# Performance work log

Hardware: AMD Instinct MI355X
Metric: run time of the kernel (lower is better)

The kernel has to match this reference:

```python
import jax, jax.numpy as jnp
import numpy as np

N_HEAD = 16
N_KV_HEAD = 8
HEAD_DIM = 128
BLOCK_SIZE = 2048


def _rope_cache(T, hd):
    # faithful to torch: freqs repeat_interleave(2) along last dim
    inv_freq = 1.0 / (10000.0 ** (jnp.arange(0, hd, 2, dtype=jnp.float32) / hd))
    t = jnp.arange(T, dtype=jnp.float32)
    freqs = jnp.outer(t, inv_freq)            # [T, hd/2]
    freqs = jnp.repeat(freqs, 2, axis=-1)     # [T, hd]
    return jnp.cos(freqs), jnp.sin(freqs)


def _apply_rope(x, cos, sin):
    # x: [B, H, T, hd]; rotate-half convention from the torch code
    hd = x.shape[-1]
    x1, x2 = x[..., : hd // 2], x[..., hd // 2 :]
    x_rot = jnp.concatenate([-x2, x1], axis=-1)
    return x * cos + x_rot * sin


def setup_inputs() -> dict:
    key = jax.random.key(0)
    ks = jax.random.split(key, 5)
    B, T, C = 4, 2048, 2048
    kv_dim = N_KV_HEAD * HEAD_DIM
    s = 0.02
    return {
        "x": jax.random.normal(ks[0], (B, T, C), dtype=jnp.float32),
        "Wq": jax.random.normal(ks[1], (C, C), dtype=jnp.float32) * s,
        "Wk": jax.random.normal(ks[2], (kv_dim, C), dtype=jnp.float32) * s,
        "Wv": jax.random.normal(ks[3], (kv_dim, C), dtype=jnp.float32) * s,
        "Wo": jax.random.normal(ks[4], (C, C), dtype=jnp.float32) * s,
    }


def reference(x, Wq, Wk, Wv, Wo):
    B, T, C = x.shape
    hd = HEAD_DIM
    # projections (torch Linear: x @ W.T)
    q = (x @ Wq.T).reshape(B, T, N_HEAD, hd).transpose(0, 2, 1, 3)      # [B,H,T,hd]
    k = (x @ Wk.T).reshape(B, T, N_KV_HEAD, hd).transpose(0, 2, 1, 3)   # [B,Hkv,T,hd]
    v = (x @ Wv.T).reshape(B, T, N_KV_HEAD, hd).transpose(0, 2, 1, 3)

    cos, sin = _rope_cache(T, hd)  # start_pos = 0
    q = _apply_rope(q, cos, sin)
    k = _apply_rope(k, cos, sin)

    # GQA: repeat kv heads
    rep = N_HEAD // N_KV_HEAD
    k = jnp.repeat(k, rep, axis=1)  # [B,H,T,hd]
    v = jnp.repeat(v, rep, axis=1)

    scale = 1.0 / jnp.sqrt(jnp.float32(hd))
    scores = jnp.einsum("bhqd,bhkd->bhqk", q, k) * scale
    causal = jnp.tril(jnp.ones((T, T), dtype=bool))
    scores = jnp.where(causal, scores, jnp.finfo(scores.dtype).min)
    attn = jax.nn.softmax(scores, axis=-1)
    out = jnp.einsum("bhqk,bhkd->bhqd", attn, v)  # [B,H,T,hd]

    y = out.transpose(0, 2, 1, 3).reshape(B, T, C)
    return y @ Wo.T
```

## Files before the change

kernel.cpp:

```cpp
#include <hip/hip_runtime.h>

#define SCALE 0.08838834764831845f

typedef unsigned short bfu;
typedef __attribute__((ext_vector_type(8))) short bf16x8;
typedef __attribute__((ext_vector_type(4))) float f32x4;
typedef __attribute__((ext_vector_type(16))) float f32x16;

__device__ __forceinline__ unsigned short f2bf(float f) {
  unsigned int u = __float_as_uint(f);
  u += 0x7FFFu + ((u >> 16) & 1u);
  return (unsigned short)(u >> 16);
}
__device__ __forceinline__ float bf2f(unsigned short h) {
  return __uint_as_float(((unsigned int)h) << 16);
}
__device__ __forceinline__ unsigned int cvtpk(float a, float b) {
  unsigned int r;
  asm("v_cvt_pk_bf16_f32 %0, %1, %2" : "=v"(r) : "v"(a), "v"(b));
  return r;
}
__device__ __forceinline__ void async16(const void* g, void* l) {
  __builtin_amdgcn_global_load_lds(
      (const __attribute__((address_space(1))) unsigned int*)g,
      (__attribute__((address_space(3))) unsigned int*)l, 16, 0, 0);
}
__device__ __forceinline__ void barrier_sb() {
  __builtin_amdgcn_sched_barrier(0);
  __builtin_amdgcn_s_barrier();
  __builtin_amdgcn_sched_barrier(0);
}
__device__ __forceinline__ void wait4_bar() {
  __builtin_amdgcn_sched_barrier(0);
  asm volatile("s_waitcnt vmcnt(4)" ::: "memory");
  __builtin_amdgcn_s_barrier();
  __builtin_amdgcn_sched_barrier(0);
}
__device__ __forceinline__ void wait0_bar() {
  __builtin_amdgcn_sched_barrier(0);
  asm volatile("s_waitcnt vmcnt(0)" ::: "memory");
  __builtin_amdgcn_s_barrier();
  __builtin_amdgcn_sched_barrier(0);
}

__global__ __launch_bounds__(256) void cvt_bf16(const float* __restrict__ src,
                                                bfu* __restrict__ dst, int n4) {
  int i = blockIdx.x * 256 + threadIdx.x;
  if (i >= n4) return;
  float4 v = ((const float4*)src)[i];
  ushort4 o;
  o.x = f2bf(v.x); o.y = f2bf(v.y); o.z = f2bf(v.z); o.w = f2bf(v.w);
  ((ushort4*)dst)[i] = o;
}

__global__ __launch_bounds__(256) void rope_table(float2* __restrict__ tab) {
  int idx = blockIdx.x * 256 + threadIdx.x;
  int t = idx >> 6, f = idx & 63;
  const float nl = -0.14391156463f;
  float th = (float)t * expf((float)f * nl);
  tab[idx] = make_float2(cosf(th), sinf(th));
}

__device__ __forceinline__ void storeC(float* p, float v) { *p = v; }
__device__ __forceinline__ void storeC(bfu* p, float v) { *p = f2bf(v); }

template <typename OutT, bool FUSE>
__global__ __launch_bounds__(512, 2) void gemm256(
    const bfu* __restrict__ A, const bfu* __restrict__ B,
    OutT* __restrict__ C, const float2* __restrict__ ropeTab,
    bfu* __restrict__ qTo, bfu* __restrict__ kTo, bfu* __restrict__ vTo,
    int M, int N, int K) {
  __shared__ __align__(16) char smem[131072];
  const int tid = threadIdx.x;
  const int w = tid >> 6, l = tid & 63;
  const int lr = l & 15, lg = l >> 4;
  const int wr = w >> 2, wc = w & 3;

  const int nwg = gridDim.x * gridDim.y;
  const int flat = blockIdx.y * gridDim.x + blockIdx.x;
  const int swz = (flat & 7) * (nwg >> 3) + (flat >> 3);
  const int m0 = (swz % gridDim.x) * 256;
  const int n0 = (swz / gridDim.x) * 256;

  const int sr = l >> 3;
  const int sc = (l & 7) ^ sr;
  auto stageHalf = [&](const bfu* G, int grow0, int kcol, char* lds) {
#pragma unroll
    for (int j = 0; j < 2; j++) {
      int row = (j * 8 + w) * 8 + sr;
      async16(G + (size_t)(grow0 + row) * K + kcol + sc * 8,
              lds + (j * 8 + w) * 1024 + l * 16);
    }
  };

  f32x4 acc[8][4];
#pragma unroll
  for (int i = 0; i < 8; i++)
#pragma unroll
    for (int j = 0; j < 4; j++) acc[i][j] = (f32x4){0.f, 0.f, 0.f, 0.f};

  stageHalf(A, m0, 0, smem);
  stageHalf(A, m0 + 128, 0, smem + 16384);
  stageHalf(B, n0, 0, smem + 65536);
  stageHalf(B, n0 + 128, 0, smem + 65536 + 16384);

  const int KT = K >> 6;
  const int swiz = (lr & 7) << 4;
  const int cbase = (wc >> 1) * 128 + (wc & 1) * 32;
#pragma unroll 1
  for (int t = 0; t < KT; t++) {
    const int bt = t & 1;
    const char* Ah = smem + bt * 32768 + wr * 16384;
    const char* Bt = smem + 65536 + bt * 32768;
    char* An = smem + (bt ^ 1) * 32768;
    char* Bn = smem + 65536 + (bt ^ 1) * 32768;
    const bool pfch = (t + 1 < KT);
    const int kn = (t + 1) << 6;

    if (pfch) {
      stageHalf(A, m0, kn, An);
      asm volatile("s_waitcnt vmcnt(2)" ::: "memory");
    } else {
      asm volatile("s_waitcnt vmcnt(0)" ::: "memory");
    }
    barrier_sb();

    bf16x8 bfr[4][2];
#pragma unroll
    for (int n = 0; n < 4; n++) {
      const char* rowp =
          Bt + (cbase + (n & 1) * 16 + (n >> 1) * 64 + lr) * 128;
#pragma unroll
      for (int s = 0; s < 2; s++)
        bfr[n][s] = *(const bf16x8*)(rowp + ((((s << 2) + lg) << 4) ^ swiz));
    }

#pragma unroll
    for (int p = 0; p < 4; p++) {
      bf16x8 af[2][2];
#pragma unroll
      for (int m2 = 0; m2 < 2; m2++) {
        const char* rowp = Ah + ((p * 2 + m2) * 16 + lr) * 128;
#pragma unroll
        for (int s = 0; s < 2; s++)
          af[m2][s] = *(const bf16x8*)(rowp + ((((s << 2) + lg) << 4) ^ swiz));
      }
      if (pfch) {
        if (p == 1) stageHalf(A, m0 + 128, kn, An + 16384);
        if (p == 2) stageHalf(B, n0, kn, Bn);
        if (p == 3) stageHalf(B, n0 + 128, kn, Bn + 16384);
      }
      __builtin_amdgcn_s_setprio(1);
#pragma unroll
      for (int m2 = 0; m2 < 2; m2++)
#pragma unroll
        for (int n = 0; n < 4; n++)
#pragma unroll
          for (int s = 0; s < 2; s++)
            acc[p * 2 + m2][n] = __builtin_amdgcn_mfma_f32_16x16x32_bf16(
                af[m2][s], bfr[n][s], acc[p * 2 + m2][n], 0, 0, 0);
      __builtin_amdgcn_s_setprio(0);
    }
    barrier_sb();
  }

  if constexpr (!FUSE) {
#pragma unroll
    for (int i = 0; i < 8; i++)
#pragma unroll
      for (int j = 0; j < 4; j++)
#pragma unroll
        for (int r = 0; r < 4; r++) {
          int gm = m0 + wr * 128 + i * 16 + lg * 4 + r;
          int gn = n0 + cbase + (j & 1) * 16 + (j >> 1) * 64 + lr;
          storeC(&C[(size_t)gm * N + gn], acc[i][j][r]);
        }
  } else {
    const int head = (n0 >> 7) + (wc >> 1);
    if (head < 24) {
#pragma unroll
      for (int i = 0; i < 8; i++)
#pragma unroll
        for (int r = 0; r < 4; r++) {
          int gm = m0 + wr * 128 + i * 16 + lg * 4 + r;
          int tt = gm & 2047, bb = gm >> 11;
          bfu* rowp = (head < 16)
                          ? qTo + (((size_t)((bb * 16 + head) * 2048 + tt)) << 7)
                          : kTo + (((size_t)((bb * 8 + head - 16) * 2048 + tt)) << 7);
          const float2* trow = ropeTab + tt * 64;
#pragma unroll
          for (int n = 0; n < 2; n++) {
            int d = (wc & 1) * 32 + n * 16 + lr;
            int i1 = d >> 1;
            float2 cs1 = trow[i1];
            float2 cs2 = trow[i1 + 32];
            float x1 = acc[i][n][r], x2 = acc[i][n + 2][r];
            rowp[d] = f2bf(x1 * cs1.x - x2 * cs1.y);
            rowp[d + 64] = f2bf(x2 * cs2.x + x1 * cs2.y);
          }
        }
    } else {
      const int kh = head - 24;
#pragma unroll
      for (int i = 0; i < 8; i++) {
        int gm0 = m0 + wr * 128 + i * 16 + lg * 4;
        int t0 = gm0 & 2047, bb = gm0 >> 11;
#pragma unroll
        for (int n = 0; n < 4; n++) {
          int d = (wc & 1) * 32 + (n & 1) * 16 + (n >> 1) * 64 + lr;
          bfu* p = vTo + (((size_t)((bb * 8 + kh) * 128 + d)) << 11) + t0;
          ushort4 o;
          o.x = f2bf(acc[i][n][0]);
          o.y = f2bf(acc[i][n][1]);
          o.z = f2bf(acc[i][n][2]);
          o.w = f2bf(acc[i][n][3]);
          *(ushort4*)p = o;
        }
      }
    }
  }
}

__global__ __launch_bounds__(256, 3) void flash_attn5(const bfu* __restrict__ qT,
                                                      const bfu* __restrict__ kT,
                                                      const bfu* __restrict__ vT,
                                                      bfu* __restrict__ attn) {
  __shared__ __align__(16) char smem[49152];
  const int tid = threadIdx.x;
  const int w = tid >> 6, l = tid & 63;
  const int ln = l & 31, h2 = l >> 5;
  const int idx = blockIdx.x;
  const int khb = idx & 31;
  const int hs = (idx >> 5) & 1;
  const int qt = 15 - (idx >> 6);
  const int kh = khb & 7, b = khb >> 3;
  const int hh = kh * 2 + hs;
  const int NT = 2 * qt + 2;
  const int qrow0 = qt * 128 + w * 32;
  const int myrow = qrow0 + ln;

  const bfu* Qh = qT + ((size_t)(b * 16 + hh) * 2048) * 128;
  const bfu* Kb = kT + ((size_t)(b * 8 + kh) * 2048) * 128;
  const bfu* Vb = vT + ((size_t)(b * 8 + kh) * 128) * 2048;

  auto stageK = [&](int kbuf, int t) {
    char* Kl = smem + kbuf * 16384;
    const bfu* src = Kb + (size_t)t * 64 * 128;
#pragma unroll
    for (int ii = 0; ii < 4; ii++) {
      int i = w * 4 + ii;
      int row = i * 4 + (l >> 4);
      int ck = (l & 15) ^ (row & 15);
      async16(src + row * 128 + ck * 8, Kl + i * 1024 + l * 16);
    }
  };
  auto stageV = [&](int t) {
    char* Vl = smem + 32768;
    const bfu* src = Vb + t * 64;
#pragma unroll
    for (int jj = 0; jj < 4; jj++) {
      int j = w * 4 + jj;
      int row = j * 8 + (l >> 3);
      int ck = (l & 7) ^ (row & 7);
      async16(src + (size_t)row * 2048 + ck * 8, Vl + j * 1024 + l * 16);
    }
  };

  bf16x8 qf[8];
#pragma unroll
  for (int dt = 0; dt < 8; dt++)
    qf[dt] = *(const bf16x8*)(Qh + (size_t)myrow * 128 + dt * 16 + h2 * 8);

  f32x16 O[4];
#pragma unroll
  for (int mt = 0; mt < 4; mt++)
#pragma unroll
    for (int r = 0; r < 16; r++) O[mt][r] = 0.f;
  float li = 0.f;

  stageK(0, 0);
  stageV(0);
  wait4_bar();

  int kb = 0;
#pragma unroll 1
  for (int t = 0; t < NT; t++) {
    const bool pf = (t + 1 < NT);
    if (pf) stageK(kb ^ 1, t + 1);

    const int k0 = t * 64;
    const bool active = k0 <= qrow0 + 31;
    bf16x8 pfr[4];

    if (active) {
      const char* Kl = smem + kb * 16384;
      f32x16 S0, S1;
#pragma unroll
      for (int r = 0; r < 16; r++) { S0[r] = 0.f; S1[r] = 0.f; }
      const int swk = (ln & 15) << 4;
      __builtin_amdgcn_s_setprio(1);
#pragma unroll
      for (int dt = 0; dt < 8; dt++) {
        bf16x8 kf0 =
            *(const bf16x8*)(Kl + ln * 256 + ((dt * 32 + h2 * 16) ^ swk));
        bf16x8 kf1 = *(const bf16x8*)(Kl + (32 + ln) * 256 +
                                      ((dt * 32 + h2 * 16) ^ swk));
        S0 = __builtin_amdgcn_mfma_f32_32x32x16_bf16(kf0, qf[dt], S0, 0, 0, 0);
        S1 = __builtin_amdgcn_mfma_f32_32x32x16_bf16(kf1, qf[dt], S1, 0, 0, 0);
      }
      __builtin_amdgcn_s_setprio(0);

      const bool need_mask = (k0 + 63) > qrow0;
#pragma unroll
      for (int half = 0; half < 2; half++) {
        float p[16];
#pragma unroll
        for (int r = 0; r < 16; r++) {
          float s = half ? S1[r] : S0[r];
          float pv = __builtin_exp2f(fmaf(s, 0.12751743f, -17.312340f));
          if (need_mask) {
            int key = k0 + half * 32 + (r & 3) + 8 * (r >> 2) + 4 * h2;
            if (key > myrow) pv = 0.f;
          }
          p[r] = pv;
          li += pv;
        }
#pragma unroll
        for (int kt = 0; kt < 2; kt++) {
          const float* q = p + kt * 8;
          unsigned int lo0 = cvtpk(q[0], q[1]);
          unsigned int lo1 = cvtpk(q[2], q[3]);
          unsigned int hi0 = cvtpk(q[4], q[5]);
          unsigned int hi1 = cvtpk(q[6], q[7]);
          unsigned int plo0 = __shfl_xor((int)lo0, 32);
          unsigned int plo1 = __shfl_xor((int)lo1, 32);
          unsigned int phi0 = __shfl_xor((int)hi0, 32);
          unsigned int phi1 = __shfl_xor((int)hi1, 32);
          union { unsigned int u[4]; bf16x8 v; } c;
          c.u[0] = h2 ? phi0 : lo0;
          c.u[1] = h2 ? phi1 : lo1;
          c.u[2] = h2 ? hi0 : plo0;
          c.u[3] = h2 ? hi1 : plo1;
          pfr[half * 2 + kt] = c.v;
        }
      }
    }

    if (pf) wait4_bar(); else wait0_bar();

    if (active) {
      const char* Vl = smem + 32768;
      const int swv = (ln & 7) << 4;
      __builtin_amdgcn_s_setprio(1);
#pragma unroll
      for (int mt = 0; mt < 4; mt++) {
        const char* vb = Vl + (mt * 32 + ln) * 128;
#pragma unroll
        for (int kt = 0; kt < 4; kt++) {
          bf16x8 vf = *(const bf16x8*)(vb + ((kt * 32 + h2 * 16) ^ swv));
          O[mt] = __builtin_amdgcn_mfma_f32_32x32x16_bf16(vf, pfr[kt], O[mt], 0, 0, 0);
        }
      }
      __builtin_amdgcn_s_setprio(0);
    }

    if (pf) {
      wait0_bar();
      stageV(t + 1);
    }
    kb ^= 1;
  }

  li += __shfl_xor(li, 32);
  const float inv = 1.f / li;
  bfu* orow = attn + ((size_t)(b * 2048 + qrow0 + ln)) * 2048 + hh * 128;
#pragma unroll
  for (int mt = 0; mt < 4; mt++)
#pragma unroll
    for (int g = 0; g < 4; g++) {
      unsigned int r0 = cvtpk(O[mt][g * 4 + 0] * inv, O[mt][g * 4 + 1] * inv);
      unsigned int r1 = cvtpk(O[mt][g * 4 + 2] * inv, O[mt][g * 4 + 3] * inv);
      uint2 o; o.x = r0; o.y = r1;
      *(uint2*)(orow + mt * 32 + g * 8 + h2 * 4) = o;
    }
}

extern "C" void kernel_launch(void* const* d_in, const int* in_sizes, int n_in,
                              void* d_out, int out_size, void* d_ws, size_t ws_size,
                              hipStream_t stream) {
  const float* x = (const float*)d_in[0];
  const float* Wq = (const float*)d_in[1];
  const float* Wk = (const float*)d_in[2];
  const float* Wv = (const float*)d_in[3];
  const float* Wo = (const float*)d_in[4];
  float* out = (float*)d_out;
  char* ws = (char*)d_ws;

  bfu* xb     = (bfu*)(ws);
  bfu* Wqkv   = (bfu*)(ws + 33554432);
  bfu* Wob    = (bfu*)(ws + 50331648);
  float2* tab = (float2*)(ws + 58720256);
  bfu* qT     = (bfu*)(ws + 125829120);
  bfu* kT     = (bfu*)(ws + 159383552);
  bfu* vT     = (bfu*)(ws + 176160768);
  bfu* attn = xb;

  cvt_bf16<<<16384, 256, 0, stream>>>(x, xb, 4194304);
  cvt_bf16<<<4096, 256, 0, stream>>>(Wq, Wqkv, 1048576);
  cvt_bf16<<<2048, 256, 0, stream>>>(Wk, Wqkv + (size_t)2048 * 2048, 524288);
  cvt_bf16<<<2048, 256, 0, stream>>>(Wv, Wqkv + (size_t)3072 * 2048, 524288);
  cvt_bf16<<<4096, 256, 0, stream>>>(Wo, Wob, 1048576);
  rope_table<<<512, 256, 0, stream>>>(tab);

  gemm256<bfu, true><<<dim3(32, 16), 512, 0, stream>>>(
      xb, Wqkv, (bfu*)nullptr, tab, qT, kT, vT, 8192, 4096, 2048);
  flash_attn5<<<1024, 256, 0, stream>>>(qT, kT, vT, attn);
  gemm256<float, false><<<dim3(32, 8), 512, 0, stream>>>(
      attn, Wob, out, nullptr, nullptr, nullptr, nullptr, 8192, 2048, 2048);
}
```

Before: 488.9 us.

## Pair causal q-tiles per block and share K/V tiles across both GQA heads

The attention kernel now uses 512-thread blocks in which both query heads of a KV group share each staged K/V tile. Each block processes q-tile pg and then q-tile 15-pg back to back, which evens out the causal work so every block runs 34 iterations. K and V are now double-buffered together and refilled with a single wait/barrier per iteration. The lane-32 shuffles are replaced with v_permlane32_swap. The changes target redundant K/V loads, causal load imbalance and synchronisation stalls, at the cost of more LDS per block and only 256 blocks in the grid.

After: 453.5 us. -7.2%, faster.

```diff
diff --git a/kernel.cpp b/kernel.cpp
--- a/kernel.cpp
+++ b/kernel.cpp
@@ -20,6 +20,9 @@
   asm("v_cvt_pk_bf16_f32 %0, %1, %2" : "=v"(r) : "v"(a), "v"(b));
   return r;
 }
+__device__ __forceinline__ void pl32swap(unsigned int& a, unsigned int& b) {
+  asm volatile("v_permlane32_swap_b32 %0, %1" : "+v"(a), "+v"(b));
+}
 __device__ __forceinline__ void async16(const void* g, void* l) {
   __builtin_amdgcn_global_load_lds(
       (const __attribute__((address_space(1))) unsigned int*)g,
@@ -27,12 +30,6 @@
 }
 __device__ __forceinline__ void barrier_sb() {
   __builtin_amdgcn_sched_barrier(0);
-  __builtin_amdgcn_s_barrier();
-  __builtin_amdgcn_sched_barrier(0);
-}
-__device__ __forceinline__ void wait4_bar() {
-  __builtin_amdgcn_sched_barrier(0);
-  asm volatile("s_waitcnt vmcnt(4)" ::: "memory");
   __builtin_amdgcn_s_barrier();
   __builtin_amdgcn_sched_barrier(0);
 }
@@ -221,55 +218,56 @@
   }
 }
 
-__global__ __launch_bounds__(256, 3) void flash_attn5(const bfu* __restrict__ qT,
+__global__ __launch_bounds__(512, 2) void flash_attn7(const bfu* __restrict__ qT,
                                                       const bfu* __restrict__ kT,
                                                       const bfu* __restrict__ vT,
                                                       bfu* __restrict__ attn) {
-  __shared__ __align__(16) char smem[49152];
+  __shared__ __align__(16) char smem[65536];
   const int tid = threadIdx.x;
   const int w = tid >> 6, l = tid & 63;
   const int ln = l & 31, h2 = l >> 5;
+  const int hsw = w >> 2, w4 = w & 3;
   const int idx = blockIdx.x;
   const int khb = idx & 31;
-  const int hs = (idx >> 5) & 1;
-  const int qt = 15 - (idx >> 6);
+  const int pg = idx >> 5;
   const int kh = khb & 7, b = khb >> 3;
-  const int hh = kh * 2 + hs;
-  const int NT = 2 * qt + 2;
-  const int qrow0 = qt * 128 + w * 32;
-  const int myrow = qrow0 + ln;
+  const int hh = kh * 2 + hsw;
+  const int nkbA = 2 * pg + 2;
+  const int NT = 34;
 
   const bfu* Qh = qT + ((size_t)(b * 16 + hh) * 2048) * 128;
   const bfu* Kb = kT + ((size_t)(b * 8 + kh) * 2048) * 128;
   const bfu* Vb = vT + ((size_t)(b * 8 + kh) * 128) * 2048;
 
-  auto stageK = [&](int kbuf, int t) {
-    char* Kl = smem + kbuf * 16384;
+  auto stageK = [&](int buf, int t) {
+    char* Kl = smem + buf * 16384;
     const bfu* src = Kb + (size_t)t * 64 * 128;
 #pragma unroll
-    for (int ii = 0; ii < 4; ii++) {
-      int i = w * 4 + ii;
+    for (int ii = 0; ii < 2; ii++) {
+      int i = w * 2 + ii;
       int row = i * 4 + (l >> 4);
       int ck = (l & 15) ^ (row & 15);
       async16(src + row * 128 + ck * 8, Kl + i * 1024 + l * 16);
     }
   };
-  auto stageV = [&](int t) {
-    char* Vl = smem + 32768;
+  auto stageV = [&](int buf, int t) {
+    char* Vl = smem + 32768 + buf * 16384;
     const bfu* src = Vb + t * 64;
 #pragma unroll
-    for (int jj = 0; jj < 4; jj++) {
-      int j = w * 4 + jj;
+    for (int jj = 0; jj < 2; jj++) {
+      int j = w * 2 + jj;
       int row = j * 8 + (l >> 3);
       int ck = (l & 7) ^ (row & 7);
       async16(src + (size_t)row * 2048 + ck * 8, Vl + j * 1024 + l * 16);
     }
   };
 
+  int qrow0 = pg * 128 + w4 * 32;
+
   bf16x8 qf[8];
 #pragma unroll
   for (int dt = 0; dt < 8; dt++)
-    qf[dt] = *(const bf16x8*)(Qh + (size_t)myrow * 128 + dt * 16 + h2 * 8);
+    qf[dt] = *(const bf16x8*)(Qh + (size_t)(qrow0 + ln) * 128 + dt * 16 + h2 * 8);
 
   f32x16 O[4];
 #pragma unroll
@@ -278,22 +276,53 @@
     for (int r = 0; r < 16; r++) O[mt][r] = 0.f;
   float li = 0.f;
 
+  auto flush = [&]() {
+    float ls = li + __shfl_xor(li, 32);
+    float inv = 1.f / ls;
+    bfu* orow = attn + ((size_t)(b * 2048 + qrow0 + ln)) * 2048 + hh * 128;
+#pragma unroll
+    for (int mt = 0; mt < 4; mt++)
+#pragma unroll
+      for (int g = 0; g < 4; g++) {
+        unsigned int r0 = cvtpk(O[mt][g * 4 + 0] * inv, O[mt][g * 4 + 1] * inv);
+        unsigned int r1 = cvtpk(O[mt][g * 4 + 2] * inv, O[mt][g * 4 + 3] * inv);
+        uint2 o; o.x = r0; o.y = r1;
+        *(uint2*)(orow + mt * 32 + g * 8 + h2 * 4) = o;
+      }
+  };
+
   stageK(0, 0);
-  stageV(0);
-  wait4_bar();
-
-  int kb = 0;
+  stageV(0, 0);
+
 #pragma unroll 1
   for (int t = 0; t < NT; t++) {
-    const bool pf = (t + 1 < NT);
-    if (pf) stageK(kb ^ 1, t + 1);
-
-    const int k0 = t * 64;
-    const bool active = k0 <= qrow0 + 31;
-    bf16x8 pfr[4];
-
-    if (active) {
-      const char* Kl = smem + kb * 16384;
+    wait0_bar();
+    if (t + 1 < NT) {
+      const int kn = (t + 1 >= nkbA) ? (t + 1 - nkbA) : (t + 1);
+      stageK((t + 1) & 1, kn);
+      stageV((t + 1) & 1, kn);
+    }
+
+    if (t == nkbA) {
+      flush();
+      qrow0 = (15 - pg) * 128 + w4 * 32;
+#pragma unroll
+      for (int dt = 0; dt < 8; dt++)
+        qf[dt] =
+            *(const bf16x8*)(Qh + (size_t)(qrow0 + ln) * 128 + dt * 16 + h2 * 8);
+#pragma unroll
+      for (int mt = 0; mt < 4; mt++)
+#pragma unroll
+        for (int r = 0; r < 16; r++) O[mt][r] = 0.f;
+      li = 0.f;
+    }
+
+    const int k0 = ((t >= nkbA) ? (t - nkbA) : t) * 64;
+    const int myrow = qrow0 + ln;
+    if (k0 <= qrow0 + 31) {
+      const char* Kl = smem + (t & 1) * 16384;
+      const char* Vl = smem + 32768 + (t & 1) * 16384;
+
       f32x16 S0, S1;
 #pragma unroll
       for (int r = 0; r < 16; r++) { S0[r] = 0.f; S1[r] = 0.f; }
@@ -311,6 +340,7 @@
       __builtin_amdgcn_s_setprio(0);
 
       const bool need_mask = (k0 + 63) > qrow0;
+      bf16x8 pfr[4];
 #pragma unroll
       for (int half = 0; half < 2; half++) {
         float p[16];
@@ -328,28 +358,18 @@
 #pragma unroll
         for (int kt = 0; kt < 2; kt++) {
           const float* q = p + kt * 8;
-          unsigned int lo0 = cvtpk(q[0], q[1]);
-          unsigned int lo1 = cvtpk(q[2], q[3]);
-          unsigned int hi0 = cvtpk(q[4], q[5]);
-          unsigned int hi1 = cvtpk(q[6], q[7]);
-          unsigned int plo0 = __shfl_xor((int)lo0, 32);
-          unsigned int plo1 = __shfl_xor((int)lo1, 32);
-          unsigned int phi0 = __shfl_xor((int)hi0, 32);
-          unsigned int phi1 = __shfl_xor((int)hi1, 32);
+          unsigned int a0 = cvtpk(q[0], q[1]);
+          unsigned int a1 = cvtpk(q[2], q[3]);
+          unsigned int b0 = cvtpk(q[4], q[5]);
+          unsigned int b1 = cvtpk(q[6], q[7]);
+          pl32swap(a0, b0);
+          pl32swap(a1, b1);
           union { unsigned int u[4]; bf16x8 v; } c;
-          c.u[0] = h2 ? phi0 : lo0;
-          c.u[1] = h2 ? phi1 : lo1;
-          c.u[2] = h2 ? hi0 : plo0;
-          c.u[3] = h2 ? hi1 : plo1;
+          c.u[0] = a0; c.u[1] = a1; c.u[2] = b0; c.u[3] = b1;
           pfr[half * 2 + kt] = c.v;
         }
       }
-    }
-
-    if (pf) wait4_bar(); else wait0_bar();
-
-    if (active) {
-      const char* Vl = smem + 32768;
+
       const int swv = (ln & 7) << 4;
       __builtin_amdgcn_s_setprio(1);
 #pragma unroll
@@ -363,26 +383,9 @@
       }
       __builtin_amdgcn_s_setprio(0);
     }
-
-    if (pf) {
-      wait0_bar();
-      stageV(t + 1);
-    }
-    kb ^= 1;
   }
 
-  li += __shfl_xor(li, 32);
-  const float inv = 1.f / li;
-  bfu* orow = attn + ((size_t)(b * 2048 + qrow0 + ln)) * 2048 + hh * 128;
-#pragma unroll
-  for (int mt = 0; mt < 4; mt++)
-#pragma unroll
-    for (int g = 0; g < 4; g++) {
-      unsigned int r0 = cvtpk(O[mt][g * 4 + 0] * inv, O[mt][g * 4 + 1] * inv);
-      unsigned int r1 = cvtpk(O[mt][g * 4 + 2] * inv, O[mt][g * 4 + 3] * inv);
-      uint2 o; o.x = r0; o.y = r1;
-      *(uint2*)(orow + mt * 32 + g * 8 + h2 * 4) = o;
-    }
+  flush();
 }
 
 extern "C" void kernel_launch(void* const* d_in, const int* in_sizes, int n_in,
@@ -414,7 +417,7 @@
 
   gemm256<bfu, true><<<dim3(32, 16), 512, 0, stream>>>(
       xb, Wqkv, (bfu*)nullptr, tab, qT, kT, vT, 8192, 4096, 2048);
-  flash_attn5<<<1024, 256, 0, stream>>>(qT, kT, vT, attn);
+  flash_attn7<<<256, 512, 0, stream>>>(qT, kT, vT, attn);
   gemm256<float, false><<<dim3(32, 8), 512, 0, stream>>>(
       attn, Wob, out, nullptr, nullptr, nullptr, nullptr, 8192, 2048, 2048);
 }
```
